# Performance work log

Measured on AMD Instinct MI355X. Metric: run time of the kernel, lower is better.

## Reference

```python
import jax, jax.numpy as jnp
import numpy as np

PULL_MARGIN = 0.5
PUSH_MARGIN = 1.0
LOSS_WEIGHT = 1.0


def setup_inputs() -> dict:
    key = jax.random.key(0)
    k1, k2, k3 = jax.random.split(key, 3)
    B, C, H, W = 4, 1, 64, 96
    pred_emb = jax.random.normal(k1, (B, C, H, W), dtype=jnp.float32)
    gt_line_index = jax.random.randint(k2, (B, H, W), 0, 20, dtype=jnp.int32)
    gt_foreground_mask = jax.random.uniform(k3, (B, H, W)) < 0.3
    return {"pred_emb": pred_emb, "gt_line_index": gt_line_index,
            "gt_foreground_mask": gt_foreground_mask}


def _safe_norm(sq):
    # sqrt with zero (not NaN) gradient at 0, matching torch.norm subgradient
    safe = jnp.sqrt(jnp.where(sq > 0, sq, 1.0))
    return jnp.where(sq > 0, safe, 0.0)


def _per_sample(pred, gt, msk):
    # pred: [C,H,W] float, gt: [H,W] int, msk: [H,W] bool. P = H*W
    C = pred.shape[0]
    p = pred.reshape(C, -1)                      # [C,P]
    g = gt.reshape(-1)                           # [P]
    m = msk.reshape(-1).astype(pred.dtype)       # [P]
    pair = m[:, None] * m[None, :]               # [P,P] both-foreground mask
    sq = jnp.sum((p[:, :, None] - p[:, None, :]) ** 2, axis=0)  # [P,P]
    dist = _safe_norm(sq)
    same = jnp.where(g[:, None] == g[None, :], pair, 0.0)  # gt_square == 1 (incl diag)
    diffm = pair - same                                     # gt_square == 2
    n_same = jnp.sum(same)
    n_diff = jnp.sum(diffm)
    # pull: mean over same-line pairs of relu(dist - pull_margin); 0 if N == 0
    pull = jnp.sum(jnp.maximum(dist - PULL_MARGIN, 0.0) * same) / jnp.maximum(n_same, 1.0)
    # push: mean over diff-line pairs of relu(push_margin - dist); only if such pairs exist
    push_raw = jnp.sum(jnp.maximum(PUSH_MARGIN - dist, 0.0) * diffm) / jnp.maximum(n_diff, 1.0)
    push = jnp.where(n_diff > 0, push_raw, 0.0)
    return pull, push


def reference(pred_emb, gt_line_index, gt_foreground_mask):
    B = pred_emb.shape[0]
    pulls, pushes = jax.vmap(_per_sample)(pred_emb, gt_line_index, gt_foreground_mask)
    loss = (jnp.sum(pulls) + jnp.sum(pushes)) / B
    return loss * LOSS_WEIGHT
```

## Files before the change

kernel.cpp:

```cpp
#include <hip/hip_runtime.h>

#define B_FIXED 4
#define P_FIX   6144
#define BLOCK   256
#define NCH     (P_FIX / BLOCK)
#define GRIDX   64
#define NJ      8
#define PULL_MARGIN 0.5f
#define PUSH_MARGIN 1.0f


__device__ __forceinline__ bool read_fg(const void* mask, int mode, long idx) {
    if (mode == 0) return ((const int*)mask)[idx] != 0;
    if (mode == 1) return ((const unsigned char*)mask)[idx] != 0;
    return ((const float*)mask)[idx] != 0.0f;
}

__global__ __launch_bounds__(BLOCK)
void fused_all(const float* __restrict__ pred,
               const int*   __restrict__ gt,
               const void*  __restrict__ mask,
               unsigned int* __restrict__ partial,
               float* __restrict__ out) {
    __shared__ __align__(16) float sval[P_FIX];
    __shared__ __align__(16) int   skey[P_FIX];
    __shared__ int   swdet[2 * (BLOCK / 64)];
    __shared__ int   swavecnt[BLOCK / 64];
    __shared__ float sredp[BLOCK / 64], sredq[BLOCK / 64];
    __shared__ int   sredn[BLOCK / 64];
    __shared__ float sloss[B_FIXED];

    const int tid  = threadIdx.x;
    const int b    = blockIdx.y;
    const int wv   = tid >> 6, lane = tid & 63;
    const long base = (long)b * P_FIX;

    const unsigned int*  mw = (const unsigned int*)mask;
    const unsigned char* m8 = (const unsigned char*)mask;
    float val[NCH]; int key[NCH];
    unsigned int detA = 0, detC = 0, fgb = 0;
    #pragma unroll
    for (int k = 0; k < NCH; ++k) {
        const int idx = k * BLOCK + tid;
        const unsigned int w = mw[idx];
        detA |= (w > 1u) ? 1u : 0u;
        detC |= (w != 0u && w != 0x3f800000u) ? 1u : 0u;
        fgb  |= (m8[base + idx] != 0) ? (1u << k) : 0u;
        val[k] = pred[base + idx];
        key[k] = gt[base + idx];
    }
    const int anyA = (__ballot(detA != 0u) != 0ull) ? 1 : 0;
    const int anyC = (__ballot(detC != 0u) != 0ull) ? 1 : 0;
    if (lane == 0) { swdet[wv * 2] = anyA; swdet[wv * 2 + 1] = anyC; }
    __syncthreads();
    int fA = 0, fC = 0;
    #pragma unroll
    for (int w = 0; w < BLOCK / 64; ++w) { fA |= swdet[w * 2]; fC |= swdet[w * 2 + 1]; }
    const int mode = (!fA) ? 0 : (!fC ? 2 : 1);

    unsigned int fgm;
    if (mode == 1) {
        fgm = fgb;
    } else if (mode == 0) {
        fgm = 0;
        #pragma unroll
        for (int k = 0; k < NCH; ++k)
            fgm |= (((const int*)mask)[base + k * BLOCK + tid] != 0) ? (1u << k) : 0u;
    } else {
        fgm = 0;
        #pragma unroll
        for (int k = 0; k < NCH; ++k)
            fgm |= (((const float*)mask)[base + k * BLOCK + tid] != 0.0f) ? (1u << k) : 0u;
    }

    int cnt = 0;
    #pragma unroll
    for (int k = 0; k < NCH; ++k)
        cnt += (int)__popcll(__ballot((fgm >> k) & 1u));
    if (lane == 0) swavecnt[wv] = cnt;
    __syncthreads();
    int waveoff = 0, n = 0;
    #pragma unroll
    for (int w = 0; w < BLOCK / 64; ++w) {
        const int c = swavecnt[w];
        n += c;
        if (w < wv) waveoff += c;
    }

    int running = waveoff;
    const unsigned long long lt = (1ull << lane) - 1ull;
    #pragma unroll
    for (int k = 0; k < NCH; ++k) {
        const bool f = (fgm >> k) & 1u;
        const unsigned long long bal = __ballot(f);
        const int pos = running + (int)__popcll(bal & lt);
        if (f) { sval[pos] = val[k]; skey[pos] = key[k]; }
        running += (int)__popcll(bal);
    }
    __syncthreads();

    const int nti   = (n + BLOCK - 1) / BLOCK;
    const int total = nti * NJ;
    float pull = 0.f, push = 0.f;
    int ns = 0;

    for (int t = blockIdx.x; t < total; t += GRIDX) {
        const int it = t / NJ, jt = t - it * NJ;
        const int  i  = it * BLOCK + tid;
        const bool iv = i < n;
        const float pi = iv ? sval[i] : 1e30f;
        const int   ki = iv ? skey[i] : -2;
        const int jlo = (jt == 0)      ? 0 : (int)(((long)jt * n / NJ) & ~3L);
        const int jhi = (jt == NJ - 1) ? n : (int)(((long)(jt + 1) * n / NJ) & ~3L);
        const int gve = jhi & ~3;

        const float4* sv4 = (const float4*)sval;
        const int4*   sk4 = (const int4*)skey;
        float p0 = 0.f, p1 = 0.f, q0 = 0.f, q1 = 0.f;
        int   c0 = 0, c1 = 0;
        #pragma unroll 2
        for (int g = (jlo >> 2); g < (gve >> 2); ++g) {
            const float4 v = sv4[g];
            const int4   k = sk4[g];
            {
                const float d = fabsf(pi - v.x);
                const bool  s = (ki == k.x);
                p0 += s ? fmaxf(d - PULL_MARGIN, 0.f) : 0.f;
                q0 += s ? 0.f : fmaxf(PUSH_MARGIN - d, 0.f);
                c0 += s ? 1 : 0;
            }
            {
                const float d = fabsf(pi - v.y);
                const bool  s = (ki == k.y);
                p1 += s ? fmaxf(d - PULL_MARGIN, 0.f) : 0.f;
                q1 += s ? 0.f : fmaxf(PUSH_MARGIN - d, 0.f);
                c1 += s ? 1 : 0;
            }
            {
                const float d = fabsf(pi - v.z);
                const bool  s = (ki == k.z);
                p0 += s ? fmaxf(d - PULL_MARGIN, 0.f) : 0.f;
                q0 += s ? 0.f : fmaxf(PUSH_MARGIN - d, 0.f);
                c0 += s ? 1 : 0;
            }
            {
                const float d = fabsf(pi - v.w);
                const bool  s = (ki == k.w);
                p1 += s ? fmaxf(d - PULL_MARGIN, 0.f) : 0.f;
                q1 += s ? 0.f : fmaxf(PUSH_MARGIN - d, 0.f);
                c1 += s ? 1 : 0;
            }
        }
        for (int j = gve; j < jhi; ++j) {
            const float d = fabsf(pi - sval[j]);
            const bool  s = (ki == skey[j]);
            p0 += s ? fmaxf(d - PULL_MARGIN, 0.f) : 0.f;
            q0 += s ? 0.f : fmaxf(PUSH_MARGIN - d, 0.f);
            c0 += s ? 1 : 0;
        }
        pull += p0 + p1; push += q0 + q1; ns += c0 + c1;
    }

    #pragma unroll
    for (int off = 32; off > 0; off >>= 1) {
        pull += __shfl_down(pull, off);
        push += __shfl_down(push, off);
        ns   += __shfl_down(ns,   off);
    }
    if (lane == 0) { sredp[wv] = pull; sredq[wv] = push; sredn[wv] = ns; }
    __syncthreads();
    if (tid == 0) {
        float tp = 0.f, tq = 0.f; int tn = 0;
        #pragma unroll
        for (int w = 0; w < BLOCK / 64; ++w) {
            tp += sredp[w]; tq += sredq[w]; tn += sredn[w];
        }
        unsigned int* slot = partial + (size_t)(b * GRIDX + blockIdx.x) * 4;
        __hip_atomic_store(&slot[0], __float_as_uint(tp), __ATOMIC_RELAXED,
                           __HIP_MEMORY_SCOPE_AGENT);
        __hip_atomic_store(&slot[1], __float_as_uint(tq), __ATOMIC_RELAXED,
                           __HIP_MEMORY_SCOPE_AGENT);
        __hip_atomic_store(&slot[2], (unsigned int)tn, __ATOMIC_RELAXED,
                           __HIP_MEMORY_SCOPE_AGENT);
        __hip_atomic_store(&slot[3], (unsigned int)n, __ATOMIC_RELEASE,
                           __HIP_MEMORY_SCOPE_AGENT);
    }

    if (blockIdx.x == 0 && blockIdx.y == 0) {
        unsigned int* slot = partial + (size_t)tid * 4;
        unsigned int w3;
        do { w3 = __hip_atomic_load(&slot[3], __ATOMIC_ACQUIRE,
                                    __HIP_MEMORY_SCOPE_AGENT); }
        while (w3 & 0x80000000u);
        const unsigned int w0 = __hip_atomic_load(&slot[0], __ATOMIC_RELAXED,
                                                  __HIP_MEMORY_SCOPE_AGENT);
        const unsigned int w1 = __hip_atomic_load(&slot[1], __ATOMIC_RELAXED,
                                                  __HIP_MEMORY_SCOPE_AGENT);
        const unsigned int w2 = __hip_atomic_load(&slot[2], __ATOMIC_RELAXED,
                                                  __HIP_MEMORY_SCOPE_AGENT);

        float fp = __uint_as_float(w0), fq = __uint_as_float(w1);
        int   fns = (int)w2;
        const int fn = (int)w3;
        #pragma unroll
        for (int off = 32; off > 0; off >>= 1) {
            fp  += __shfl_down(fp,  off);
            fq  += __shfl_down(fq,  off);
            fns += __shfl_down(fns, off);
        }
        if (lane == 0) {
            const long nd = (long)fn * (long)fn - (long)fns;
            const float lp = fp / (float)(fns > 1 ? fns : 1);
            const float lq = (nd > 0) ? fq / (float)nd : 0.f;
            sloss[wv] = lp + lq;
        }
        __syncthreads();
        if (tid == 0)
            out[0] = (sloss[0] + sloss[1] + sloss[2] + sloss[3])
                     * (1.0f / (float)B_FIXED);
    }
}

#define TJ 256

__device__ __forceinline__ int detect_mask_mode_g(const void* mask, int P) {
    __shared__ int s_flags[2];
    const unsigned int* mw = (const unsigned int*)mask;
    unsigned int not01 = 0, notf01 = 0;
    for (int idx = threadIdx.x; idx < P; idx += blockDim.x) {
        unsigned int w = mw[idx];
        not01  |= (w > 1u) ? 1u : 0u;
        notf01 |= (w != 0u && w != 0x3f800000u) ? 1u : 0u;
    }
    if (threadIdx.x == 0) { s_flags[0] = 0; s_flags[1] = 0; }
    __syncthreads();
    if (not01)  atomicOr(&s_flags[0], 1);
    if (notf01) atomicOr(&s_flags[1], 1);
    __syncthreads();
    int mode;
    if (!s_flags[0])      mode = 0;
    else if (!s_flags[1]) mode = 2;
    else                  mode = 1;
    return mode;
}

__global__ __launch_bounds__(BLOCK)
void fallback_pair_kernel(const float* __restrict__ pred,
                          const int*   __restrict__ gt,
                          const void*  __restrict__ mask,
                          float* __restrict__ accF, int* __restrict__ nsI,
                          int* __restrict__ npI, int C, int P) {
    extern __shared__ char smem[];
    float* sval = (float*)smem;
    int*   skey = (int*)(sval + (long)C * TJ);
    __shared__ float sred[BLOCK / 64][2];
    __shared__ int   sredi[BLOCK / 64][2];

    const int b   = blockIdx.y;
    const int tid = threadIdx.x;
    const int mode = detect_mask_mode_g(mask, P);
    const long pixBase  = (long)b * P;
    const long predBase = (long)b * C * P;

    const int  i  = blockIdx.x * BLOCK + tid;
    int ki = -2;
    if (i < P) ki = read_fg(mask, mode, pixBase + i) ? gt[pixBase + i] : -2;
    const bool ifg = (ki >= 0);

    float pull = 0.f, push = 0.f;
    int ns = 0, np = 0;

    for (int j0 = 0; j0 < P; j0 += TJ) {
        __syncthreads();
        {
            const int j = j0 + tid;
            const bool v = j < P;
            bool fg = v ? read_fg(mask, mode, pixBase + j) : false;
            for (int c = 0; c < C; ++c)
                sval[c * TJ + tid] = v ? pred[predBase + (long)c * P + j] : -1e30f;
            skey[tid] = (v && fg) ? gt[pixBase + j] : -1;
        }
        __syncthreads();
        if (i < P) {
            for (int jj = 0; jj < TJ; ++jj) {
                float sq = 0.f;
                for (int c = 0; c < C; ++c) {
                    const float d = pred[predBase + (long)c * P + i] - sval[c * TJ + jj];
                    sq = fmaf(d, d, sq);
                }
                const float dist = sqrtf(sq);
                const int   kj = skey[jj];
                const bool  pm = ifg & (kj >= 0);
                const bool  s  = (ki == kj);
                pull += s ? fmaxf(dist - PULL_MARGIN, 0.f) : 0.f;
                push += (pm && !s) ? fmaxf(PUSH_MARGIN - dist, 0.f) : 0.f;
                ns   += s ? 1 : 0;
                np   += pm ? 1 : 0;
            }
        }
    }

    #pragma unroll
    for (int off = 32; off > 0; off >>= 1) {
        pull += __shfl_down(pull, off);
        push += __shfl_down(push, off);
        ns   += __shfl_down(ns,   off);
        np   += __shfl_down(np,   off);
    }
    const int wave = tid >> 6, lane = tid & 63;
    if (lane == 0) {
        sred[wave][0] = pull; sred[wave][1] = push;
        sredi[wave][0] = ns;  sredi[wave][1] = np;
    }
    __syncthreads();
    if (tid == 0) {
        float tp = 0.f, tq = 0.f; int tn = 0, tm = 0;
        #pragma unroll
        for (int w = 0; w < BLOCK / 64; ++w) {
            tp += sred[w][0]; tq += sred[w][1];
            tn += sredi[w][0]; tm += sredi[w][1];
        }
        atomicAdd(&accF[b * 4 + 0], tp);
        atomicAdd(&accF[b * 4 + 1], tq);
        atomicAdd(&nsI[b], tn);
        atomicAdd(&npI[b], tm);
    }
}

__global__ void finalize_fallback(const float* __restrict__ accF,
                                  const int* __restrict__ nsI,
                                  const int* __restrict__ npI,
                                  float* __restrict__ out) {
    if (threadIdx.x == 0 && blockIdx.x == 0) {
        float loss = 0.f;
        #pragma unroll
        for (int b = 0; b < B_FIXED; ++b) {
            const long ns = nsI[b];
            const long nd = (long)npI[b] - ns;
            const float pull = accF[b * 4 + 0] / (float)(ns > 1 ? ns : 1);
            const float push = (nd > 0) ? accF[b * 4 + 1] / (float)nd : 0.f;
            loss += pull + push;
        }
        out[0] = loss * (1.0f / (float)B_FIXED);
    }
}

extern "C" void kernel_launch(void* const* d_in, const int* in_sizes, int n_in,
                              void* d_out, int out_size, void* d_ws, size_t ws_size,
                              hipStream_t stream) {
    const float* pred = (const float*)d_in[0];
    const int*   gt   = (const int*)d_in[1];
    const void*  mask = d_in[2];
    float* out = (float*)d_out;

    const int C = in_sizes[0] / in_sizes[1];
    const int P = in_sizes[1] / B_FIXED;

    if (C == 1 && P == P_FIX && ws_size >= 4096) {
        dim3 grid(GRIDX, B_FIXED);
        fused_all<<<grid, BLOCK, 0, stream>>>(pred, gt, mask,
                                              (unsigned int*)d_ws, out);
    } else {
        float* accF = (float*)((char*)d_ws + 4096);
        int*   nsI  = (int*)((char*)d_ws + 4096 + 128);
        int*   npI  = (int*)((char*)d_ws + 4096 + 192);
        hipMemsetAsync((char*)d_ws + 4096, 0, 512, stream);
        dim3 gF((P + BLOCK - 1) / BLOCK, B_FIXED);
        fallback_pair_kernel<<<gF, BLOCK, (size_t)(C + 1) * TJ * 4, stream>>>(
            pred, gt, mask, accF, nsI, npI, C, P);
        finalize_fallback<<<1, 64, 0, stream>>>(accF, nsI, npI, out);
    }
}
```

Baseline: 70.43 us.

## Bucket foreground pixels by line key and compute push over all pairs minus same-key correction

The kernel now builds a shared-memory histogram of gt keys and scatters foreground pixels sorted by key. The main loop computes the push term over all pairs without key comparisons, then subtracts same-key contributions and adds pull only over the pixel's own key segment. The same-pair count comes from the sum of squared histogram counts instead of per-pair counting. It also processes two i-rows per thread with NJ doubled, adds an all-zero-mask early path, and keeps a fallback full loop for out-of-range keys. The cost is extra atomics, syncs and divergent per-thread segment loops.

```diff
diff --git a/kernel.cpp b/kernel.cpp
--- a/kernel.cpp
+++ b/kernel.cpp
@@ -5,7 +5,9 @@
 #define BLOCK   256
 #define NCH     (P_FIX / BLOCK)
 #define GRIDX   64
-#define NJ      8
+#define NJ      16
+#define IBLK    2
+#define NBIN    32
 #define PULL_MARGIN 0.5f
 #define PUSH_MARGIN 1.0f
 
@@ -14,6 +16,13 @@
     if (mode == 0) return ((const int*)mask)[idx] != 0;
     if (mode == 1) return ((const unsigned char*)mask)[idx] != 0;
     return ((const float*)mask)[idx] != 0.0f;
+}
+
+__device__ __forceinline__ float relu_push(float diff) {
+    return fmaxf(PUSH_MARGIN - fabsf(diff), 0.0f);
+}
+__device__ __forceinline__ float relu_pull(float diff) {
+    return fmaxf(fabsf(diff) - PULL_MARGIN, 0.0f);
 }
 
 __global__ __launch_bounds__(BLOCK)
@@ -24,8 +33,11 @@
                float* __restrict__ out) {
     __shared__ __align__(16) float sval[P_FIX];
     __shared__ __align__(16) int   skey[P_FIX];
-    __shared__ int   swdet[2 * (BLOCK / 64)];
-    __shared__ int   swavecnt[BLOCK / 64];
+    __shared__ int   swdet[3 * (BLOCK / 64)];
+    __shared__ int   shist[NBIN];
+    __shared__ int   sboff[NBIN];
+    __shared__ int   snext[NBIN];
+    __shared__ int   smeta[3];
     __shared__ float sredp[BLOCK / 64], sredq[BLOCK / 64];
     __shared__ int   sredn[BLOCK / 64];
     __shared__ float sloss[B_FIXED];
@@ -38,28 +50,40 @@
     const unsigned int*  mw = (const unsigned int*)mask;
     const unsigned char* m8 = (const unsigned char*)mask;
     float val[NCH]; int key[NCH];
-    unsigned int detA = 0, detC = 0, fgb = 0;
+    unsigned int detA = 0, detC = 0, detN = 0, fgb = 0;
     #pragma unroll
     for (int k = 0; k < NCH; ++k) {
         const int idx = k * BLOCK + tid;
         const unsigned int w = mw[idx];
         detA |= (w > 1u) ? 1u : 0u;
         detC |= (w != 0u && w != 0x3f800000u) ? 1u : 0u;
+        detN |= w;
         fgb  |= (m8[base + idx] != 0) ? (1u << k) : 0u;
         val[k] = pred[base + idx];
         key[k] = gt[base + idx];
     }
     const int anyA = (__ballot(detA != 0u) != 0ull) ? 1 : 0;
     const int anyC = (__ballot(detC != 0u) != 0ull) ? 1 : 0;
-    if (lane == 0) { swdet[wv * 2] = anyA; swdet[wv * 2 + 1] = anyC; }
-    __syncthreads();
-    int fA = 0, fC = 0;
-    #pragma unroll
-    for (int w = 0; w < BLOCK / 64; ++w) { fA |= swdet[w * 2]; fC |= swdet[w * 2 + 1]; }
+    const int anyN = (__ballot(detN != 0u) != 0ull) ? 1 : 0;
+    if (lane == 0) {
+        swdet[wv * 3 + 0] = anyA;
+        swdet[wv * 3 + 1] = anyC;
+        swdet[wv * 3 + 2] = anyN;
+    }
+    if (tid < NBIN) shist[tid] = 0;
+    if (tid == 0)   smeta[2] = 0;
+    __syncthreads();
+    int fA = 0, fC = 0, fN = 0;
+    #pragma unroll
+    for (int w = 0; w < BLOCK / 64; ++w) {
+        fA |= swdet[w * 3 + 0]; fC |= swdet[w * 3 + 1]; fN |= swdet[w * 3 + 2];
+    }
     const int mode = (!fA) ? 0 : (!fC ? 2 : 1);
 
     unsigned int fgm;
-    if (mode == 1) {
+    if (!fN) {
+        fgm = 0;
+    } else if (mode == 1) {
         fgm = fgb;
     } else if (mode == 0) {
         fgm = 0;
@@ -73,93 +97,131 @@
             fgm |= (((const float*)mask)[base + k * BLOCK + tid] != 0.0f) ? (1u << k) : 0u;
     }
 
-    int cnt = 0;
-    #pragma unroll
-    for (int k = 0; k < NCH; ++k)
-        cnt += (int)__popcll(__ballot((fgm >> k) & 1u));
-    if (lane == 0) swavecnt[wv] = cnt;
-    __syncthreads();
-    int waveoff = 0, n = 0;
-    #pragma unroll
-    for (int w = 0; w < BLOCK / 64; ++w) {
-        const int c = swavecnt[w];
-        n += c;
-        if (w < wv) waveoff += c;
-    }
-
-    int running = waveoff;
-    const unsigned long long lt = (1ull << lane) - 1ull;
+    unsigned int badbit = 0;
     #pragma unroll
     for (int k = 0; k < NCH; ++k) {
-        const bool f = (fgm >> k) & 1u;
-        const unsigned long long bal = __ballot(f);
-        const int pos = running + (int)__popcll(bal & lt);
-        if (f) { sval[pos] = val[k]; skey[pos] = key[k]; }
-        running += (int)__popcll(bal);
-    }
-    __syncthreads();
-
-    const int nti   = (n + BLOCK - 1) / BLOCK;
+        if ((fgm >> k) & 1u) {
+            const int kk = key[k];
+            badbit |= (unsigned int)(kk < 0 || kk >= NBIN);
+            atomicAdd(&shist[kk & (NBIN - 1)], 1);
+        }
+    }
+    if (badbit) atomicOr(&smeta[2], 1);
+    __syncthreads();
+
+    if (wv == 0) {
+        const int c = (lane < NBIN) ? shist[lane] : 0;
+        int incl = c;
+        #pragma unroll
+        for (int off = 1; off < NBIN; off <<= 1) {
+            const int u = __shfl_up(incl, off);
+            if (lane >= off) incl += u;
+        }
+        int sq = c * c;
+        #pragma unroll
+        for (int off = 1; off < NBIN; off <<= 1)
+            sq += __shfl_xor(sq, off);
+        const int ntot = __shfl(incl, NBIN - 1);
+        if (lane < NBIN) { sboff[lane] = incl - c; snext[lane] = incl - c; }
+        if (lane == 0)   { smeta[0] = ntot; smeta[1] = sq; }
+    }
+    __syncthreads();
+    const int n       = smeta[0];
+    const int ns_hist = smeta[1];
+    const int badkey  = smeta[2];
+
+    #pragma unroll
+    for (int k = 0; k < NCH; ++k) {
+        if ((fgm >> k) & 1u) {
+            const int r = atomicAdd(&snext[key[k] & (NBIN - 1)], 1);
+            sval[r] = val[k]; skey[r] = key[k];
+        }
+    }
+    __syncthreads();
+
+    const int nti   = (n + IBLK * BLOCK - 1) / (IBLK * BLOCK);
     const int total = nti * NJ;
     float pull = 0.f, push = 0.f;
-    int ns = 0;
+    int cnt = 0;
 
     for (int t = blockIdx.x; t < total; t += GRIDX) {
         const int it = t / NJ, jt = t - it * NJ;
-        const int  i  = it * BLOCK + tid;
-        const bool iv = i < n;
-        const float pi = iv ? sval[i] : 1e30f;
-        const int   ki = iv ? skey[i] : -2;
+        const int i0 = it * (IBLK * BLOCK) + tid;
+        const int i1 = i0 + BLOCK;
+        const bool v0 = i0 < n, v1 = i1 < n;
+        const float pi0 = v0 ? sval[i0] : 1e30f;
+        const float pi1 = v1 ? sval[i1] : 1e30f;
+        const int   ki0 = v0 ? skey[i0] : -2;
+        const int   ki1 = v1 ? skey[i1] : -2;
         const int jlo = (jt == 0)      ? 0 : (int)(((long)jt * n / NJ) & ~3L);
         const int jhi = (jt == NJ - 1) ? n : (int)(((long)(jt + 1) * n / NJ) & ~3L);
         const int gve = jhi & ~3;
 
-        const float4* sv4 = (const float4*)sval;
-        const int4*   sk4 = (const int4*)skey;
-        float p0 = 0.f, p1 = 0.f, q0 = 0.f, q1 = 0.f;
-        int   c0 = 0, c1 = 0;
-        #pragma unroll 2
-        for (int g = (jlo >> 2); g < (gve >> 2); ++g) {
-            const float4 v = sv4[g];
-            const int4   k = sk4[g];
-            {
-                const float d = fabsf(pi - v.x);
-                const bool  s = (ki == k.x);
-                p0 += s ? fmaxf(d - PULL_MARGIN, 0.f) : 0.f;
-                q0 += s ? 0.f : fmaxf(PUSH_MARGIN - d, 0.f);
-                c0 += s ? 1 : 0;
-            }
-            {
-                const float d = fabsf(pi - v.y);
-                const bool  s = (ki == k.y);
-                p1 += s ? fmaxf(d - PULL_MARGIN, 0.f) : 0.f;
-                q1 += s ? 0.f : fmaxf(PUSH_MARGIN - d, 0.f);
-                c1 += s ? 1 : 0;
-            }
-            {
-                const float d = fabsf(pi - v.z);
-                const bool  s = (ki == k.z);
-                p0 += s ? fmaxf(d - PULL_MARGIN, 0.f) : 0.f;
-                q0 += s ? 0.f : fmaxf(PUSH_MARGIN - d, 0.f);
-                c0 += s ? 1 : 0;
-            }
-            {
-                const float d = fabsf(pi - v.w);
-                const bool  s = (ki == k.w);
-                p1 += s ? fmaxf(d - PULL_MARGIN, 0.f) : 0.f;
-                q1 += s ? 0.f : fmaxf(PUSH_MARGIN - d, 0.f);
-                c1 += s ? 1 : 0;
-            }
-        }
-        for (int j = gve; j < jhi; ++j) {
-            const float d = fabsf(pi - sval[j]);
-            const bool  s = (ki == skey[j]);
-            p0 += s ? fmaxf(d - PULL_MARGIN, 0.f) : 0.f;
-            q0 += s ? 0.f : fmaxf(PUSH_MARGIN - d, 0.f);
-            c0 += s ? 1 : 0;
-        }
-        pull += p0 + p1; push += q0 + q1; ns += c0 + c1;
-    }
+        if (!badkey) {
+            const float4* sv4 = (const float4*)sval;
+            float q0 = 0.f, q1 = 0.f, q2 = 0.f, q3 = 0.f;
+            #pragma unroll 2
+            for (int g = (jlo >> 2); g < (gve >> 2); ++g) {
+                const float4 v = sv4[g];
+                q0 += relu_push(pi0 - v.x);
+                q1 += relu_push(pi0 - v.y);
+                q0 += relu_push(pi0 - v.z);
+                q1 += relu_push(pi0 - v.w);
+                q2 += relu_push(pi1 - v.x);
+                q3 += relu_push(pi1 - v.y);
+                q2 += relu_push(pi1 - v.z);
+                q3 += relu_push(pi1 - v.w);
+            }
+            for (int j = gve; j < jhi; ++j) {
+                const float v = sval[j];
+                q0 += relu_push(pi0 - v);
+                q2 += relu_push(pi1 - v);
+            }
+            float q = (q0 + q1) + (q2 + q3);
+
+            if (v0) {
+                const int kk  = ki0 & (NBIN - 1);
+                const int slo = sboff[kk], shi = slo + shist[kk];
+                const int clo = max(slo, jlo), chi = min(shi, jhi);
+                for (int j = clo; j < chi; ++j) {
+                    const float d = pi0 - sval[j];
+                    pull += relu_pull(d);
+                    q    -= relu_push(d);
+                }
+            }
+            if (v1) {
+                const int kk  = ki1 & (NBIN - 1);
+                const int slo = sboff[kk], shi = slo + shist[kk];
+                const int clo = max(slo, jlo), chi = min(shi, jhi);
+                for (int j = clo; j < chi; ++j) {
+                    const float d = pi1 - sval[j];
+                    pull += relu_pull(d);
+                    q    -= relu_push(d);
+                }
+            }
+            push += q;
+        } else {
+            for (int j = jlo; j < jhi; ++j) {
+                const float v = sval[j]; const int kj = skey[j];
+                {
+                    const float d = fabsf(pi0 - v);
+                    const bool  s = (ki0 == kj);
+                    pull += s ? fmaxf(d - PULL_MARGIN, 0.f) : 0.f;
+                    push += s ? 0.f : fmaxf(PUSH_MARGIN - d, 0.f);
+                    cnt  += s ? 1 : 0;
+                }
+                {
+                    const float d = fabsf(pi1 - v);
+                    const bool  s = (ki1 == kj);
+                    pull += s ? fmaxf(d - PULL_MARGIN, 0.f) : 0.f;
+                    push += s ? 0.f : fmaxf(PUSH_MARGIN - d, 0.f);
+                    cnt  += s ? 1 : 0;
+                }
+            }
+        }
+    }
+
+    int ns = badkey ? cnt : ((blockIdx.x == 0 && tid == 0) ? ns_hist : 0);
 
     #pragma unroll
     for (int off = 32; off > 0; off >>= 1) {
```

After: 71.34 us. About the same (+1.3%).
